# Kernel optimization log

Measured on AMD Instinct MI355X. Metric: run time of the kernel, lower is better.

The kernel has to match this reference:

```python
import jax, jax.numpy as jnp
import numpy as np

# Model dims (Llama-7B-like GQA)
S, B, D_MODEL = 2048, 2, 4096   # total seq, batch, hidden
NH, NKV, HD = 32, 8, 128        # q heads, kv heads, head dim
TP = 4                          # ring size -> number of KV blocks
SB = S // TP                    # KV block length per ring step


def setup_inputs() -> dict:
    key = jax.random.key(0)
    k1, k2, k3 = jax.random.split(key, 3)
    hidden_states = jax.random.normal(k1, (S, B, D_MODEL), jnp.float32)
    w_qkv = jax.random.normal(k2, (D_MODEL, (NH + 2 * NKV) * HD), jnp.float32) / np.sqrt(D_MODEL)
    w_o = jax.random.normal(k3, (NH * HD, D_MODEL), jnp.float32) / np.sqrt(NH * HD)
    return {"hidden_states": hidden_states, "w_qkv": w_qkv, "w_o": w_o}


def _ring_attention(hidden_states, w_qkv, w_o):
    # fused QKV projection: [S,B,D] @ [D,(NH+2*NKV)*HD]
    qkv = hidden_states @ w_qkv
    q, k, v = jnp.split(qkv, [NH * HD, (NH + NKV) * HD], axis=-1)
    q = q.reshape(S, B, NH, HD).transpose(1, 2, 0, 3)    # [B,NH,S,HD]
    k = k.reshape(S, B, NKV, HD).transpose(1, 2, 0, 3)   # [B,NKV,S,HD]
    v = v.reshape(S, B, NKV, HD).transpose(1, 2, 0, 3)

    groups = NH // NKV  # GQA: expand kv heads to match q heads
    k = jnp.repeat(k, groups, axis=1)  # [B,NH,S,HD]
    v = jnp.repeat(v, groups, axis=1)

    scale = 1.0 / np.sqrt(HD)

    # Split K/V along sequence into TP ring blocks: [TP,B,NH,SB,HD]
    k_blocks = k.reshape(B, NH, TP, SB, HD).transpose(2, 0, 1, 3, 4)
    v_blocks = v.reshape(B, NH, TP, SB, HD).transpose(2, 0, 1, 3, 4)

    # Online-softmax (flash-attention style) accumulation over ring steps.
    m0 = jnp.full((B, NH, S), -jnp.inf, q.dtype)   # running row max
    l0 = jnp.zeros((B, NH, S), q.dtype)            # running denom
    acc0 = jnp.zeros((B, NH, S, HD), q.dtype)      # running numerator

    def step(carry, kv):
        m, l, acc = carry
        kb, vb = kv  # [B,NH,SB,HD]
        s = jnp.einsum('bhqd,bhkd->bhqk', q, kb) * scale  # [B,NH,S,SB]
        m_new = jnp.maximum(m, s.max(-1))
        p = jnp.exp(s - m_new[..., None])
        alpha = jnp.exp(m - m_new)
        l = l * alpha + p.sum(-1)
        acc = acc * alpha[..., None] + jnp.einsum('bhqk,bhkd->bhqd', p, vb)
        return (m_new, l, acc), None

    (m, l, acc), _ = jax.lax.scan(step, (m0, l0, acc0), (k_blocks, v_blocks))
    attn = acc / l[..., None]  # [B,NH,S,HD]

    # [B,NH,S,HD] -> [S*B, NH*HD] -> o_proj -> [S,B,D]
    attn = attn.transpose(2, 0, 1, 3).reshape(S * B, NH * HD)
    return (attn @ w_o).reshape(S, B, D_MODEL)


def reference(hidden_states, w_qkv, w_o):
    return _ring_attention(hidden_states, w_qkv, w_o)
```

## Files before the change

kernel.cpp:

```cpp
#include <hip/hip_runtime.h>
#include <hip/hip_bf16.h>


typedef __bf16 bf16x8 __attribute__((ext_vector_type(8)));
typedef float f32x4 __attribute__((ext_vector_type(4)));
typedef unsigned short u16;
typedef u16 u16x4 __attribute__((ext_vector_type(4)));
typedef u16 u16x8 __attribute__((ext_vector_type(8)));
typedef unsigned int u32;

#define SEQ    2048
#define BATCH  2
#define NROWS  4096
#define DM     4096
#define QKVC   6144
#define QSCALE (0.08838834764831845f * 1.4426950408889634f)

__device__ __forceinline__ u16 f2bf(float f) {
  union { float f; u32 u; } v; v.f = f;
  u32 r = v.u + 0x7fffu + ((v.u >> 16) & 1u);
  return (u16)(r >> 16);
}

__device__ __forceinline__ void gload16(const void* g, void* l) {
  __builtin_amdgcn_global_load_lds(
      (const __attribute__((address_space(1))) unsigned int*)g,
      (__attribute__((address_space(3))) unsigned int*)l, 16, 0, 0);
}

__global__ __launch_bounds__(256) void conv_f32_bf16(
    const float* __restrict__ in, u16* __restrict__ out) {
  size_t i = ((size_t)blockIdx.x * 256 + threadIdx.x) * 8;
  float4 a = *(const float4*)(in + i);
  float4 b = *(const float4*)(in + i + 4);
  u16x8 o;
  o[0] = f2bf(a.x); o[1] = f2bf(a.y); o[2] = f2bf(a.z); o[3] = f2bf(a.w);
  o[4] = f2bf(b.x); o[5] = f2bf(b.y); o[6] = f2bf(b.z); o[7] = f2bf(b.w);
  *(u16x8*)(out + i) = o;
}

__global__ __launch_bounds__(256) void transpose_f32_bf16(
    const float* __restrict__ in, u16* __restrict__ out, int K, int N) {
  __shared__ u16 tile[64][65];
  const int k0 = blockIdx.y * 64, n0 = blockIdx.x * 64;
  const int t = threadIdx.x;
#pragma unroll
  for (int i = 0; i < 4; ++i) {
    int slot = i * 256 + t;
    int r = slot >> 4, cq = slot & 15;
    float4 v = *(const float4*)(in + (size_t)(k0 + r) * N + n0 + cq * 4);
    tile[cq * 4 + 0][r] = f2bf(v.x);
    tile[cq * 4 + 1][r] = f2bf(v.y);
    tile[cq * 4 + 2][r] = f2bf(v.z);
    tile[cq * 4 + 3][r] = f2bf(v.w);
  }
  __syncthreads();
#pragma unroll
  for (int i = 0; i < 2; ++i) {
    int slot = i * 256 + t;
    int n = slot >> 3, q = slot & 7;
    u16x8 o;
#pragma unroll
    for (int e = 0; e < 8; ++e) o[e] = tile[n][q * 8 + e];
    *(u16x8*)(out + (size_t)(n0 + n) * K + k0 + q * 8) = o;
  }
}

__global__ __launch_bounds__(256) void vtrans(
    const u16* __restrict__ qkv, u16* __restrict__ vt) {
  __shared__ u16 tile[64][66];
  const int s0 = blockIdx.x * 64, d0 = blockIdx.y * 64;
  const int z = blockIdx.z;
  const int b = z >> 3, kvh = z & 7;
  const int t = threadIdx.x;
#pragma unroll
  for (int i = 0; i < 2; ++i) {
    int chunk = i * 256 + t;
    int r = chunk >> 3, q = chunk & 7;
    u16x8 v = *(const u16x8*)&qkv[(size_t)((s0 + r) * 2 + b) * QKVC + 5120 + kvh * 128 + d0 + q * 8];
#pragma unroll
    for (int e = 0; e < 8; ++e) tile[r][q * 8 + e] = v[e];
  }
  __syncthreads();
#pragma unroll
  for (int i = 0; i < 2; ++i) {
    int chunk = i * 256 + t;
    int d = chunk >> 3, q = chunk & 7;
    u16x8 o;
#pragma unroll
    for (int e = 0; e < 8; ++e) o[e] = tile[q * 8 + e][d];
    *(u16x8*)&vt[(size_t)(z * 128 + d0 + d) * SEQ + s0 + q * 8] = o;
  }
}

template <int CBF16, int SCALEQ>
__global__ __launch_bounds__(256) void gemm_bt(
    const u16* __restrict__ A, const u16* __restrict__ B,
    void* __restrict__ C, int M, int N, int K) {
  __shared__ u16 As[128 * 64];
  __shared__ u16 Bs[128 * 64];
  const int t = threadIdx.x;
  const int w = t >> 6, lane = t & 63;
  const int g = lane >> 4, c = lane & 15;
  const int m0 = blockIdx.y * 128, n0 = blockIdx.x * 128;
  const int wm = w >> 1, wn = w & 1;

  const f32x4 fz = {0.f, 0.f, 0.f, 0.f};
  f32x4 acc[4][4];
#pragma unroll
  for (int mi = 0; mi < 4; ++mi)
#pragma unroll
    for (int ni = 0; ni < 4; ++ni) acc[mi][ni] = fz;

  int srow[4], sgq[4];
#pragma unroll
  for (int j = 0; j < 4; ++j) {
    int slot = (j * 4 + w) * 64 + lane;
    srow[j] = slot >> 3;
    sgq[j] = (slot & 7) ^ (srow[j] & 7);
  }

  auto stage = [&](int kt) {
#pragma unroll
    for (int j = 0; j < 4; ++j) {
      int base = (j * 4 + w) * 64;
      gload16(A + (size_t)(m0 + srow[j]) * K + kt * 64 + sgq[j] * 8, &As[base * 8]);
      gload16(B + (size_t)(n0 + srow[j]) * K + kt * 64 + sgq[j] * 8, &Bs[base * 8]);
    }
  };

  const int nkt = K >> 6;
  stage(0);
  for (int kt = 0; kt < nkt; ++kt) {
    __syncthreads();
    bf16x8 af[4][2], bfr[4][2];
#pragma unroll
    for (int mi = 0; mi < 4; ++mi)
#pragma unroll
      for (int kk = 0; kk < 2; ++kk) {
        int q2 = (kk * 4 + g) ^ (c & 7);
        af[mi][kk] = *(const bf16x8*)&As[(wm * 64 + mi * 16 + c) * 64 + q2 * 8];
        bfr[mi][kk] = *(const bf16x8*)&Bs[(wn * 64 + mi * 16 + c) * 64 + q2 * 8];
      }
#pragma unroll
    for (int kk = 0; kk < 2; ++kk)
#pragma unroll
      for (int mi = 0; mi < 4; ++mi)
#pragma unroll
        for (int ni = 0; ni < 4; ++ni)
          acc[mi][ni] = __builtin_amdgcn_mfma_f32_16x16x32_bf16(
              af[mi][kk], bfr[ni][kk], acc[mi][ni], 0, 0, 0);
    __syncthreads();
    if (kt + 1 < nkt) stage(kt + 1);
  }

#pragma unroll
  for (int mi = 0; mi < 4; ++mi)
#pragma unroll
    for (int ni = 0; ni < 4; ++ni) {
      int row = m0 + wm * 64 + mi * 16 + g * 4;
      int col = n0 + wn * 64 + ni * 16 + c;
      float sc = (SCALEQ && col < 4096) ? QSCALE : 1.0f;
#pragma unroll
      for (int r = 0; r < 4; ++r) {
        float x = acc[mi][ni][r] * sc;
        if (CBF16) ((u16*)C)[(size_t)(row + r) * N + col] = f2bf(x);
        else       ((float*)C)[(size_t)(row + r) * N + col] = x;
      }
    }
}

__global__ __launch_bounds__(512, 4) void attn_fwd2(
    const u16* __restrict__ qkv, const u16* __restrict__ vtg,
    u16* __restrict__ out) {
  __shared__ u16 Ks[2][64 * 128];
  __shared__ u16 Vs[2][128 * 64];
  __shared__ u16 Ps[8][16 * 64];
  const int t = threadIdx.x;
  const int w = t >> 6, lane = t & 63;
  const int g = lane >> 4, c = lane & 15;
  const int bh = blockIdx.y;
  const int b = bh >> 5, h = bh & 31, kvh = h >> 2;
  const int q0 = blockIdx.x * 128 + w * 16;

  bf16x8 qf[4];
#pragma unroll
  for (int kk = 0; kk < 4; ++kk)
    qf[kk] = *(const bf16x8*)&qkv[(size_t)((q0 + c) * 2 + b) * QKVC + h * 128 + kk * 32 + g * 8];

  const f32x4 fz = {0.f, 0.f, 0.f, 0.f};
  f32x4 acc[8];
#pragma unroll
  for (int db = 0; db < 8; ++db) acc[db] = fz;
  float m_ = -__builtin_inff(), l_ = 0.f;

  const int w4g = w * 4 + g;
  const u16* pK = qkv + (size_t)b * QKVC + 4096 + kvh * 128 + (size_t)((c ^ w4g) & 15) * 8;
  const int vrow = w * 8 + (lane >> 3);
  const u16* pV = vtg + (size_t)(b * 8 + kvh) * 128 * SEQ + (size_t)((lane & 7) ^ (lane >> 3)) * 8;

  auto stage = [&](int bufi, int kv0) {
#pragma unroll
    for (int j = 0; j < 2; ++j)
      gload16(pK + (size_t)(kv0 + j * 32 + w4g) * (2 * QKVC), &Ks[bufi][(j * 8 + w) * 512]);
#pragma unroll
    for (int j = 0; j < 2; ++j)
      gload16(pV + (size_t)(j * 64 + vrow) * SEQ + kv0, &Vs[bufi][(j * 8 + w) * 512]);
  };

  stage(0, 0);
  int buf = 0;
  for (int kv0 = 0; kv0 < SEQ; kv0 += 64) {
    __syncthreads();
    if (kv0 + 64 < SEQ) stage(buf ^ 1, kv0 + 64);

    f32x4 st[4];
    __builtin_amdgcn_s_setprio(1);
#pragma unroll
    for (int kf = 0; kf < 4; ++kf) {
      const u16* kr = &Ks[buf][(kf * 16 + c) * 128];
      bf16x8 kfr[4];
#pragma unroll
      for (int kk = 0; kk < 4; ++kk)
        kfr[kk] = *(const bf16x8*)&kr[(((kk * 4 + g) ^ c) & 15) * 8];
      f32x4 s = fz;
#pragma unroll
      for (int kk = 0; kk < 4; ++kk)
        s = __builtin_amdgcn_mfma_f32_16x16x32_bf16(kfr[kk], qf[kk], s, 0, 0, 0);
      st[kf] = s;
    }
    __builtin_amdgcn_s_setprio(0);

    float mloc = st[0][0];
#pragma unroll
    for (int kf = 0; kf < 4; ++kf)
#pragma unroll
      for (int r = 0; r < 4; ++r) mloc = fmaxf(mloc, st[kf][r]);
    mloc = fmaxf(mloc, __shfl_xor(mloc, 16));
    mloc = fmaxf(mloc, __shfl_xor(mloc, 32));
    if (!__all(mloc - m_ <= 8.0f)) {
      float mnew = fmaxf(m_, mloc);
      float alpha = __builtin_amdgcn_exp2f(m_ - mnew);
      l_ *= alpha;
      f32x4 av;
#pragma unroll
      for (int r = 0; r < 4; ++r) av[r] = __shfl(alpha, g * 4 + r);
#pragma unroll
      for (int db = 0; db < 8; ++db) acc[db] *= av;
      m_ = mnew;
    }
    float ps = 0.f;
#pragma unroll
    for (int kf = 0; kf < 4; ++kf) {
      u16x4 pk;
#pragma unroll
      for (int r = 0; r < 4; ++r) {
        float p = __builtin_amdgcn_exp2f(st[kf][r] - m_);
        ps += p;
        pk[r] = f2bf(p);
      }
      *(u16x4*)&Ps[w][c * 64 + ((((kf * 2 + (g >> 1)) ^ (c & 7)) << 3) | ((g & 1) << 2))] = pk;
    }
    ps += __shfl_xor(ps, 16);
    ps += __shfl_xor(ps, 32);
    l_ += ps;

    bf16x8 pa0 = *(const bf16x8*)&Ps[w][c * 64 + (((0 + g) ^ (c & 7)) << 3)];
    bf16x8 pa1 = *(const bf16x8*)&Ps[w][c * 64 + (((4 + g) ^ (c & 7)) << 3)];
    __builtin_amdgcn_s_setprio(1);
#pragma unroll
    for (int db = 0; db < 8; ++db) {
      const u16* vr = &Vs[buf][(db * 16 + c) * 64];
      bf16x8 v0 = *(const bf16x8*)&vr[(((0 + g) ^ (c & 7)) << 3)];
      bf16x8 v1 = *(const bf16x8*)&vr[(((4 + g) ^ (c & 7)) << 3)];
      acc[db] = __builtin_amdgcn_mfma_f32_16x16x32_bf16(pa0, v0, acc[db], 0, 0, 0);
      acc[db] = __builtin_amdgcn_mfma_f32_16x16x32_bf16(pa1, v1, acc[db], 0, 0, 0);
    }
    __builtin_amdgcn_s_setprio(0);
    buf ^= 1;
  }

  float linv = __builtin_amdgcn_rcpf(l_);
  f32x4 il;
#pragma unroll
  for (int r = 0; r < 4; ++r) il[r] = __shfl(linv, g * 4 + r);
#pragma unroll
  for (int db = 0; db < 8; ++db) {
#pragma unroll
    for (int r = 0; r < 4; ++r) {
      int s = q0 + g * 4 + r;
      out[(size_t)(s * 2 + b) * DM + h * 128 + db * 16 + c] = f2bf(acc[db][r] * il[r]);
    }
  }
}

extern "C" void kernel_launch(void* const* d_in, const int* in_sizes, int n_in,
                              void* d_out, int out_size, void* d_ws, size_t ws_size,
                              hipStream_t stream) {
  const float* hidden = (const float*)d_in[0];
  const float* w_qkv  = (const float*)d_in[1];
  const float* w_o    = (const float*)d_in[2];
  float* outp = (float*)d_out;

  const size_t SZ_X  = (size_t)NROWS * DM * 2;
  const size_t SZ_WQ = (size_t)QKVC * DM * 2;
  const size_t SZ_WO = (size_t)DM * DM * 2;
  const size_t SZ_QKV = (size_t)NROWS * QKVC * 2;
  if (ws_size < SZ_X + SZ_WQ + SZ_WO + SZ_QKV) return;

  char* ws = (char*)d_ws;
  u16* Xb    = (u16*)ws;
  u16* WqkvT = (u16*)(ws + SZ_X);
  u16* WoT   = (u16*)(ws + SZ_X + SZ_WQ);
  u16* QKVb  = (u16*)(ws + SZ_X + SZ_WQ + SZ_WO);
  u16* VtG   = WqkvT;
  u16* Attn  = Xb;

  conv_f32_bf16<<<(NROWS * (size_t)DM) / 2048, 256, 0, stream>>>(hidden, Xb);
  transpose_f32_bf16<<<dim3(QKVC / 64, DM / 64), 256, 0, stream>>>(w_qkv, WqkvT, DM, QKVC);
  transpose_f32_bf16<<<dim3(DM / 64, DM / 64), 256, 0, stream>>>(w_o, WoT, DM, DM);
  gemm_bt<1, 1><<<dim3(QKVC / 128, NROWS / 128), 256, 0, stream>>>(Xb, WqkvT, QKVb, NROWS, QKVC, DM);
  vtrans<<<dim3(SEQ / 64, 2, 16), 256, 0, stream>>>(QKVb, VtG);
  attn_fwd2<<<dim3(SEQ / 128, BATCH * 32), 512, 0, stream>>>(QKVb, VtG, Attn);
  gemm_bt<0, 0><<<dim3(DM / 128, NROWS / 128), 256, 0, stream>>>(Attn, WoT, outp, NROWS, DM, DM);
}
```

Measured before the change: 616.8 us.

## Replace 128x128 GEMM with 256x256 double-buffered 8-wave pipelined GEMM

```diff
diff --git a/kernel.cpp b/kernel.cpp
--- a/kernel.cpp
+++ b/kernel.cpp
@@ -26,6 +26,12 @@
   __builtin_amdgcn_global_load_lds(
       (const __attribute__((address_space(1))) unsigned int*)g,
       (__attribute__((address_space(3))) unsigned int*)l, 16, 0, 0);
+}
+
+__device__ __forceinline__ void wg_barrier() {
+  __builtin_amdgcn_sched_barrier(0);
+  __builtin_amdgcn_s_barrier();
+  __builtin_amdgcn_sched_barrier(0);
 }
 
 __global__ __launch_bounds__(256) void conv_f32_bf16(
@@ -94,76 +100,153 @@
 }
 
 template <int CBF16, int SCALEQ>
-__global__ __launch_bounds__(256) void gemm_bt(
+__global__ __launch_bounds__(512, 2) void gemm256(
     const u16* __restrict__ A, const u16* __restrict__ B,
-    void* __restrict__ C, int M, int N, int K) {
-  __shared__ u16 As[128 * 64];
-  __shared__ u16 Bs[128 * 64];
+    void* __restrict__ C, int M, int N, int K, int nby) {
+  __shared__ u16 As[2 * 2 * 8192];
+  __shared__ u16 Bs[2 * 2 * 8192];
   const int t = threadIdx.x;
-  const int w = t >> 6, lane = t & 63;
-  const int g = lane >> 4, c = lane & 15;
-  const int m0 = blockIdx.y * 128, n0 = blockIdx.x * 128;
-  const int wm = w >> 1, wn = w & 1;
+  const int w = t >> 6, l = t & 63;
+  const int g = l >> 4, c = l & 15;
+  const int wm = w >> 2, wn = w & 3;
+
+  const int nwg = gridDim.x;
+  const int sid = (blockIdx.x & 7) * (nwg >> 3) + (blockIdx.x >> 3);
+  const int by = sid % nby, bx = sid / nby;
+  const int m0 = by * 256, n0 = bx * 256;
+
+  const int gsrc = (l & 7) ^ (l >> 3);
+  const u16* pA = A + (size_t)(m0 + w * 8 + (l >> 3)) * K + gsrc * 8;
+  const u16* pB = B + (size_t)(n0 + w * 8 + (l >> 3)) * K + gsrc * 8;
+
+#define STG_A(h, tt) do { int d_ = (tt) & 1;                                    \
+    gload16(pA + (size_t)((h) * 128) * K + (tt) * 64,                           \
+            &As[(d_ * 2 + (h)) * 8192 + w * 512]);                              \
+    gload16(pA + (size_t)((h) * 128 + 64) * K + (tt) * 64,                      \
+            &As[(d_ * 2 + (h)) * 8192 + 4096 + w * 512]); } while (0)
+#define STG_B(h, tt) do { int d_ = (tt) & 1;                                    \
+    gload16(pB + (size_t)((h) * 128) * K + (tt) * 64,                           \
+            &Bs[(d_ * 2 + (h)) * 8192 + w * 512]);                              \
+    gload16(pB + (size_t)((h) * 128 + 64) * K + (tt) * 64,                      \
+            &Bs[(d_ * 2 + (h)) * 8192 + 4096 + w * 512]); } while (0)
+
+  const u16* aRd = &As[wm * 8192 + c * 64];
+  const u16* bRd = &Bs[(wn >> 1) * 8192 + ((wn & 1) * 64 + c) * 64];
+  const int xr0 = ((0 + g) ^ (c & 7)) << 3;
+  const int xr1 = ((4 + g) ^ (c & 7)) << 3;
 
   const f32x4 fz = {0.f, 0.f, 0.f, 0.f};
-  f32x4 acc[4][4];
-#pragma unroll
-  for (int mi = 0; mi < 4; ++mi)
-#pragma unroll
-    for (int ni = 0; ni < 4; ++ni) acc[mi][ni] = fz;
-
-  int srow[4], sgq[4];
-#pragma unroll
-  for (int j = 0; j < 4; ++j) {
-    int slot = (j * 4 + w) * 64 + lane;
-    srow[j] = slot >> 3;
-    sgq[j] = (slot & 7) ^ (srow[j] & 7);
-  }
-
-  auto stage = [&](int kt) {
-#pragma unroll
-    for (int j = 0; j < 4; ++j) {
-      int base = (j * 4 + w) * 64;
-      gload16(A + (size_t)(m0 + srow[j]) * K + kt * 64 + sgq[j] * 8, &As[base * 8]);
-      gload16(B + (size_t)(n0 + srow[j]) * K + kt * 64 + sgq[j] * 8, &Bs[base * 8]);
-    }
-  };
+  f32x4 acc[8][4];
+#pragma unroll
+  for (int mi = 0; mi < 8; ++mi)
+#pragma unroll
+    for (int nj = 0; nj < 4; ++nj) acc[mi][nj] = fz;
 
   const int nkt = K >> 6;
-  stage(0);
-  for (int kt = 0; kt < nkt; ++kt) {
-    __syncthreads();
-    bf16x8 af[4][2], bfr[4][2];
-#pragma unroll
-    for (int mi = 0; mi < 4; ++mi)
-#pragma unroll
-      for (int kk = 0; kk < 2; ++kk) {
-        int q2 = (kk * 4 + g) ^ (c & 7);
-        af[mi][kk] = *(const bf16x8*)&As[(wm * 64 + mi * 16 + c) * 64 + q2 * 8];
-        bfr[mi][kk] = *(const bf16x8*)&Bs[(wn * 64 + mi * 16 + c) * 64 + q2 * 8];
-      }
+  STG_A(0, 0); STG_A(1, 0); STG_B(0, 0); STG_B(1, 0);
+  STG_B(0, 1); STG_B(1, 1);
+  asm volatile("s_waitcnt vmcnt(4)" ::: "memory");
+  __builtin_amdgcn_sched_barrier(0);
+  wg_barrier();
+
+  for (int tt = 0; tt < nkt; ++tt) {
+    const int d = tt & 1;
+    const u16* aT = aRd + d * 16384;
+    const u16* bT = bRd + d * 16384;
+    bf16x8 av[4][2], b01[2][2], b23[2][2];
+
+#pragma unroll
+    for (int m = 0; m < 4; ++m) {
+      av[m][0] = *(const bf16x8*)(aT + m * 1024 + xr0);
+      av[m][1] = *(const bf16x8*)(aT + m * 1024 + xr1);
+    }
+#pragma unroll
+    for (int n = 0; n < 2; ++n) {
+      b01[n][0] = *(const bf16x8*)(bT + n * 1024 + xr0);
+      b01[n][1] = *(const bf16x8*)(bT + n * 1024 + xr1);
+    }
+    if (tt + 1 < nkt) STG_A(0, tt + 1);
+    wg_barrier();
+    __builtin_amdgcn_s_setprio(1);
 #pragma unroll
     for (int kk = 0; kk < 2; ++kk)
 #pragma unroll
-      for (int mi = 0; mi < 4; ++mi)
-#pragma unroll
-        for (int ni = 0; ni < 4; ++ni)
-          acc[mi][ni] = __builtin_amdgcn_mfma_f32_16x16x32_bf16(
-              af[mi][kk], bfr[ni][kk], acc[mi][ni], 0, 0, 0);
-    __syncthreads();
-    if (kt + 1 < nkt) stage(kt + 1);
-  }
-
-#pragma unroll
-  for (int mi = 0; mi < 4; ++mi)
-#pragma unroll
-    for (int ni = 0; ni < 4; ++ni) {
-      int row = m0 + wm * 64 + mi * 16 + g * 4;
-      int col = n0 + wn * 64 + ni * 16 + c;
+      for (int m = 0; m < 4; ++m)
+#pragma unroll
+        for (int n = 0; n < 2; ++n)
+          acc[m][n] = __builtin_amdgcn_mfma_f32_16x16x32_bf16(
+              av[m][kk], b01[n][kk], acc[m][n], 0, 0, 0);
+    __builtin_amdgcn_s_setprio(0);
+    wg_barrier();
+
+#pragma unroll
+    for (int n = 0; n < 2; ++n) {
+      b23[n][0] = *(const bf16x8*)(bT + (2 + n) * 1024 + xr0);
+      b23[n][1] = *(const bf16x8*)(bT + (2 + n) * 1024 + xr1);
+    }
+    if (tt + 1 < nkt) STG_A(1, tt + 1);
+    wg_barrier();
+    __builtin_amdgcn_s_setprio(1);
+#pragma unroll
+    for (int kk = 0; kk < 2; ++kk)
+#pragma unroll
+      for (int m = 0; m < 4; ++m)
+#pragma unroll
+        for (int n = 0; n < 2; ++n)
+          acc[m][2 + n] = __builtin_amdgcn_mfma_f32_16x16x32_bf16(
+              av[m][kk], b23[n][kk], acc[m][2 + n], 0, 0, 0);
+    __builtin_amdgcn_s_setprio(0);
+    wg_barrier();
+
+#pragma unroll
+    for (int m = 0; m < 4; ++m) {
+      av[m][0] = *(const bf16x8*)(aT + (4 + m) * 1024 + xr0);
+      av[m][1] = *(const bf16x8*)(aT + (4 + m) * 1024 + xr1);
+    }
+    if (tt + 2 < nkt) STG_B(0, tt + 2);
+    wg_barrier();
+    __builtin_amdgcn_s_setprio(1);
+#pragma unroll
+    for (int kk = 0; kk < 2; ++kk)
+#pragma unroll
+      for (int m = 0; m < 4; ++m)
+#pragma unroll
+        for (int n = 0; n < 2; ++n)
+          acc[4 + m][2 + n] = __builtin_amdgcn_mfma_f32_16x16x32_bf16(
+              av[m][kk], b23[n][kk], acc[4 + m][2 + n], 0, 0, 0);
+    __builtin_amdgcn_s_setprio(0);
+    wg_barrier();
+
+    if (tt + 2 < nkt) STG_B(1, tt + 2);
+    if (tt < nkt - 2) asm volatile("s_waitcnt vmcnt(4)" ::: "memory");
+    else              asm volatile("s_waitcnt vmcnt(0)" ::: "memory");
+    __builtin_amdgcn_sched_barrier(0);
+    wg_barrier();
+    __builtin_amdgcn_s_setprio(1);
+#pragma unroll
+    for (int kk = 0; kk < 2; ++kk)
+#pragma unroll
+      for (int m = 0; m < 4; ++m)
+#pragma unroll
+        for (int n = 0; n < 2; ++n)
+          acc[4 + m][n] = __builtin_amdgcn_mfma_f32_16x16x32_bf16(
+              av[m][kk], b01[n][kk], acc[4 + m][n], 0, 0, 0);
+    __builtin_amdgcn_s_setprio(0);
+    wg_barrier();
+  }
+#undef STG_A
+#undef STG_B
+
+#pragma unroll
+  for (int mi = 0; mi < 8; ++mi)
+#pragma unroll
+    for (int nj = 0; nj < 4; ++nj) {
+      int row = m0 + wm * 128 + mi * 16 + g * 4;
+      int col = n0 + wn * 64 + nj * 16 + c;
       float sc = (SCALEQ && col < 4096) ? QSCALE : 1.0f;
 #pragma unroll
       for (int r = 0; r < 4; ++r) {
-        float x = acc[mi][ni][r] * sc;
+        float x = acc[mi][nj][r] * sc;
         if (CBF16) ((u16*)C)[(size_t)(row + r) * N + col] = f2bf(x);
         else       ((float*)C)[(size_t)(row + r) * N + col] = x;
       }
@@ -319,8 +402,8 @@
   conv_f32_bf16<<<(NROWS * (size_t)DM) / 2048, 256, 0, stream>>>(hidden, Xb);
   transpose_f32_bf16<<<dim3(QKVC / 64, DM / 64), 256, 0, stream>>>(w_qkv, WqkvT, DM, QKVC);
   transpose_f32_bf16<<<dim3(DM / 64, DM / 64), 256, 0, stream>>>(w_o, WoT, DM, DM);
-  gemm_bt<1, 1><<<dim3(QKVC / 128, NROWS / 128), 256, 0, stream>>>(Xb, WqkvT, QKVb, NROWS, QKVC, DM);
+  gemm256<1, 1><<<(QKVC / 256) * (NROWS / 256), 512, 0, stream>>>(Xb, WqkvT, QKVb, NROWS, QKVC, DM, NROWS / 256);
   vtrans<<<dim3(SEQ / 64, 2, 16), 256, 0, stream>>>(QKVb, VtG);
   attn_fwd2<<<dim3(SEQ / 128, BATCH * 32), 512, 0, stream>>>(QKVb, VtG, Attn);
-  gemm_bt<0, 0><<<dim3(DM / 128, NROWS / 128), 256, 0, stream>>>(Attn, WoT, outp, NROWS, DM, DM);
-}
+  gemm256<0, 0><<<(DM / 256) * (NROWS / 256), 512, 0, stream>>>(Attn, WoT, outp, NROWS, DM, DM, NROWS / 256);
+}
```

Measured after the change: 574.5 us. -6.9%, faster.

## Replace GEMM with double-buffered 8-wave kernel, larger N tiles, XCD-aware block mapping

Applied to the files above, without the earlier changes.

```diff
diff --git a/kernel.cpp b/kernel.cpp
--- a/kernel.cpp
+++ b/kernel.cpp
@@ -93,77 +93,99 @@
   }
 }
 
-template <int CBF16, int SCALEQ>
-__global__ __launch_bounds__(256) void gemm_bt(
+template <int NJ, int CBF16, int SCALEQ>
+__global__ __launch_bounds__(512, 2) void gemm_np(
     const u16* __restrict__ A, const u16* __restrict__ B,
-    void* __restrict__ C, int M, int N, int K) {
-  __shared__ u16 As[128 * 64];
-  __shared__ u16 Bs[128 * 64];
+    void* __restrict__ C, int M, int N, int K, int nby) {
+  __shared__ u16 As[2 * 8192];
+  __shared__ u16 Bs[2 * NJ * 4096];
   const int t = threadIdx.x;
-  const int w = t >> 6, lane = t & 63;
-  const int g = lane >> 4, c = lane & 15;
-  const int m0 = blockIdx.y * 128, n0 = blockIdx.x * 128;
-  const int wm = w >> 1, wn = w & 1;
+  const int w = t >> 6, l = t & 63;
+  const int g = l >> 4, c = l & 15;
+  const int wm = w >> 2, wn = w & 3;
+
+  const int nwg = gridDim.x;
+  const int sid = (blockIdx.x & 7) * (nwg >> 3) + (blockIdx.x >> 3);
+  const int by = sid % nby, bx = sid / nby;
+  const int m0 = by * 128, n0 = bx * (NJ * 64);
+
+  const int gsrc = (l & 7) ^ (l >> 3);
+  const u16* pA = A + (size_t)(m0 + w * 8 + (l >> 3)) * K + gsrc * 8;
+  const u16* pB = B + (size_t)(n0 + w * 8 + (l >> 3)) * K + gsrc * 8;
+
+  auto stage = [&](int tt) {
+    const int dn = tt & 1;
+#pragma unroll
+    for (int u = 0; u < 2; ++u)
+      gload16(pA + (size_t)(u * 64) * K + tt * 64,
+              &As[dn * 8192 + u * 4096 + w * 512]);
+#pragma unroll
+    for (int u = 0; u < NJ; ++u)
+      gload16(pB + (size_t)(u * 64) * K + tt * 64,
+              &Bs[dn * NJ * 4096 + u * 4096 + w * 512]);
+  };
+
+  const int xr0 = ((0 + g) ^ (c & 7)) << 3;
+  const int xr1 = ((4 + g) ^ (c & 7)) << 3;
 
   const f32x4 fz = {0.f, 0.f, 0.f, 0.f};
-  f32x4 acc[4][4];
-#pragma unroll
-  for (int mi = 0; mi < 4; ++mi)
-#pragma unroll
-    for (int ni = 0; ni < 4; ++ni) acc[mi][ni] = fz;
-
-  int srow[4], sgq[4];
-#pragma unroll
-  for (int j = 0; j < 4; ++j) {
-    int slot = (j * 4 + w) * 64 + lane;
-    srow[j] = slot >> 3;
-    sgq[j] = (slot & 7) ^ (srow[j] & 7);
-  }
-
-  auto stage = [&](int kt) {
-#pragma unroll
-    for (int j = 0; j < 4; ++j) {
-      int base = (j * 4 + w) * 64;
-      gload16(A + (size_t)(m0 + srow[j]) * K + kt * 64 + sgq[j] * 8, &As[base * 8]);
-      gload16(B + (size_t)(n0 + srow[j]) * K + kt * 64 + sgq[j] * 8, &Bs[base * 8]);
-    }
-  };
+  f32x4 acc[4][NJ];
+#pragma unroll
+  for (int m = 0; m < 4; ++m)
+#pragma unroll
+    for (int n = 0; n < NJ; ++n) acc[m][n] = fz;
 
   const int nkt = K >> 6;
   stage(0);
-  for (int kt = 0; kt < nkt; ++kt) {
-    __syncthreads();
-    bf16x8 af[4][2], bfr[4][2];
-#pragma unroll
-    for (int mi = 0; mi < 4; ++mi)
-#pragma unroll
-      for (int kk = 0; kk < 2; ++kk) {
-        int q2 = (kk * 4 + g) ^ (c & 7);
-        af[mi][kk] = *(const bf16x8*)&As[(wm * 64 + mi * 16 + c) * 64 + q2 * 8];
-        bfr[mi][kk] = *(const bf16x8*)&Bs[(wn * 64 + mi * 16 + c) * 64 + q2 * 8];
-      }
-#pragma unroll
-    for (int kk = 0; kk < 2; ++kk)
-#pragma unroll
-      for (int mi = 0; mi < 4; ++mi)
-#pragma unroll
-        for (int ni = 0; ni < 4; ++ni)
-          acc[mi][ni] = __builtin_amdgcn_mfma_f32_16x16x32_bf16(
-              af[mi][kk], bfr[ni][kk], acc[mi][ni], 0, 0, 0);
-    __syncthreads();
-    if (kt + 1 < nkt) stage(kt + 1);
-  }
-
-#pragma unroll
-  for (int mi = 0; mi < 4; ++mi)
-#pragma unroll
-    for (int ni = 0; ni < 4; ++ni) {
-      int row = m0 + wm * 64 + mi * 16 + g * 4;
-      int col = n0 + wn * 64 + ni * 16 + c;
+  asm volatile("s_waitcnt vmcnt(0)" ::: "memory");
+  __builtin_amdgcn_s_barrier();
+
+  for (int tt = 0; tt < nkt; ++tt) {
+    const int d = tt & 1;
+    if (tt + 1 < nkt) stage(tt + 1);
+
+    const u16* aT = &As[d * 8192 + (wm * 64 + c) * 64];
+    const u16* bT = &Bs[d * NJ * 4096 + (wn * NJ * 16 + c) * 64];
+    bf16x8 av[4][2], bv[NJ][2];
+#pragma unroll
+    for (int m = 0; m < 4; ++m) {
+      av[m][0] = *(const bf16x8*)(aT + m * 1024 + xr0);
+      av[m][1] = *(const bf16x8*)(aT + m * 1024 + xr1);
+    }
+#pragma unroll
+    for (int n = 0; n < NJ; ++n) {
+      bv[n][0] = *(const bf16x8*)(bT + n * 1024 + xr0);
+      bv[n][1] = *(const bf16x8*)(bT + n * 1024 + xr1);
+    }
+
+#pragma unroll
+    for (int h = 0; h < NJ / 2; ++h) {
+      if (h) __builtin_amdgcn_s_barrier();
+      __builtin_amdgcn_s_setprio(1);
+#pragma unroll
+      for (int kk = 0; kk < 2; ++kk)
+#pragma unroll
+        for (int m = 0; m < 4; ++m)
+#pragma unroll
+          for (int n = 0; n < 2; ++n)
+            acc[m][2 * h + n] = __builtin_amdgcn_mfma_f32_16x16x32_bf16(
+                av[m][kk], bv[2 * h + n][kk], acc[m][2 * h + n], 0, 0, 0);
+      __builtin_amdgcn_s_setprio(0);
+    }
+    asm volatile("s_waitcnt vmcnt(0)" ::: "memory");
+    __builtin_amdgcn_s_barrier();
+  }
+
+#pragma unroll
+  for (int m = 0; m < 4; ++m)
+#pragma unroll
+    for (int n = 0; n < NJ; ++n) {
+      int row = m0 + wm * 64 + m * 16 + g * 4;
+      int col = n0 + wn * (NJ * 16) + n * 16 + c;
       float sc = (SCALEQ && col < 4096) ? QSCALE : 1.0f;
 #pragma unroll
       for (int r = 0; r < 4; ++r) {
-        float x = acc[mi][ni][r] * sc;
+        float x = acc[m][n][r] * sc;
         if (CBF16) ((u16*)C)[(size_t)(row + r) * N + col] = f2bf(x);
         else       ((float*)C)[(size_t)(row + r) * N + col] = x;
       }
@@ -319,8 +341,8 @@
   conv_f32_bf16<<<(NROWS * (size_t)DM) / 2048, 256, 0, stream>>>(hidden, Xb);
   transpose_f32_bf16<<<dim3(QKVC / 64, DM / 64), 256, 0, stream>>>(w_qkv, WqkvT, DM, QKVC);
   transpose_f32_bf16<<<dim3(DM / 64, DM / 64), 256, 0, stream>>>(w_o, WoT, DM, DM);
-  gemm_bt<1, 1><<<dim3(QKVC / 128, NROWS / 128), 256, 0, stream>>>(Xb, WqkvT, QKVb, NROWS, QKVC, DM);
+  gemm_np<6, 1, 1><<<512, 512, 0, stream>>>(Xb, WqkvT, QKVb, NROWS, QKVC, DM, 32);
   vtrans<<<dim3(SEQ / 64, 2, 16), 256, 0, stream>>>(QKVb, VtG);
   attn_fwd2<<<dim3(SEQ / 128, BATCH * 32), 512, 0, stream>>>(QKVb, VtG, Attn);
-  gemm_bt<0, 0><<<dim3(DM / 128, NROWS / 128), 256, 0, stream>>>(Attn, WoT, outp, NROWS, DM, DM);
-}
+  gemm_np<4, 0, 0><<<512, 512, 0, stream>>>(Attn, WoT, outp, NROWS, DM, DM, 32);
+}
```

Result: slower. 691.3 us (+12.1%).
